# Optimization experiments

Hardware: AMD Instinct MI355X
Metric: run time of the kernel (lower is better)

The kernel has to match this reference:

```python
import jax, jax.numpy as jnp
import numpy as np
import math

B, L, D, H = 4, 1024, 1024, 16
HD = D // H

def setup_inputs() -> dict:
    rng = jax.random.key(0)
    ks = jax.random.split(rng, 11)
    def lin(k):
        # orthogonal-ish init not needed for numerics; normal scaled like torch default
        return jax.random.normal(k, (D, D), dtype=jnp.float32) * 0.02
    return {
        'key':   jax.random.normal(ks[0], (B, L, D), dtype=jnp.float32),
        'value': jax.random.normal(ks[1], (B, L, D), dtype=jnp.float32),
        'query': jax.random.normal(ks[2], (B, L, D), dtype=jnp.float32),
        'Wk': lin(ks[3]), 'bk': jnp.zeros((D,), jnp.float32),
        'Wq': lin(ks[4]), 'bq': jnp.zeros((D,), jnp.float32),
        'Wv': lin(ks[5]), 'bv': jnp.zeros((D,), jnp.float32),
        'Wp': lin(ks[6]), 'bp': jnp.zeros((D,), jnp.float32),
    }

def reference(key, value, query, Wk, bk, Wq, bq, Wv, bv, Wp, bp):
    # linear projections (torch Linear: x @ W.T + b)
    k = (key   @ Wk.T + bk).reshape(B, L, H, HD).transpose(0, 2, 1, 3)  # [B,H,L,hd]
    q = (query @ Wq.T + bq).reshape(B, L, H, HD).transpose(0, 2, 1, 3)
    v = (value @ Wv.T + bv).reshape(B, L, H, HD).transpose(0, 2, 1, 3)
    att = jnp.einsum('bhqd,bhkd->bhqk', q, k) * (1.0 / math.sqrt(HD))  # [B,H,L,L]
    causal = jnp.tril(jnp.ones((L, L), dtype=bool))
    att = jnp.where(causal[None, None], att, -jnp.inf)
    att = jax.nn.softmax(att, axis=-1)
    y = jnp.einsum('bhqk,bhkd->bhqd', att, v)  # [B,H,L,hd]
    y = y.transpose(0, 2, 1, 3).reshape(B, L, D)
    return y @ Wp.T + bp
```

## Files before the change

### kernel.cpp

```cpp
#include <hip/hip_runtime.h>

typedef unsigned short u16;
typedef __attribute__((ext_vector_type(8))) short bf16x8;
typedef __attribute__((ext_vector_type(4))) float f32x4;
typedef __attribute__((ext_vector_type(4))) unsigned short u16x4;

#define MFMA16 __builtin_amdgcn_mfma_f32_16x16x32_bf16

__device__ inline u16 f2bf(float f) {
    union { float f; unsigned u; } v; v.f = f;
    return (u16)((v.u + 0x8000u) >> 16);
}

__device__ inline void gld16(const u16* g, u16* l) {
    __builtin_amdgcn_global_load_lds(
        (const __attribute__((address_space(1))) unsigned int*)g,
        (__attribute__((address_space(3))) unsigned int*)l, 16, 0, 0);
}

struct CvtArgs { const float* src[7]; u16* dst[7]; };

__global__ __launch_bounds__(256) void cvt_kernel(CvtArgs a) {
    const int bid = blockIdx.x;
    int z, local;
    if (bid < 6144) { z = bid >> 11; local = bid & 2047; }
    else            { z = 3 + ((bid - 6144) >> 9); local = (bid - 6144) & 511; }
    const size_t i = ((size_t)local * 256 + threadIdx.x) * 8;
    const float* s = a.src[z];
    float4 v0 = *(const float4*)(s + i);
    float4 v1 = *(const float4*)(s + i + 4);
    union { u16 h[8]; bf16x8 v; } o;
    o.h[0] = f2bf(v0.x); o.h[1] = f2bf(v0.y); o.h[2] = f2bf(v0.z); o.h[3] = f2bf(v0.w);
    o.h[4] = f2bf(v1.x); o.h[5] = f2bf(v1.y); o.h[6] = f2bf(v1.z); o.h[7] = f2bf(v1.w);
    *(bf16x8*)(a.dst[z] + i) = o.v;
}

struct GemmArgs { const u16* A; const u16* W; const float* bias; void* out; int epi; };
struct Gemm3Args { GemmArgs g[3]; };

__global__ __launch_bounds__(256, 3) void gemm_qkv(Gemm3Args ga) {
    __shared__ u16 lA[128 * 64];
    __shared__ u16 lB[128 * 64];
    const GemmArgs g = ga.g[blockIdx.z];
    const int t = threadIdx.x, wave = t >> 6, lane = t & 63;
    const int quad = lane >> 4, l16 = lane & 15;
    const int bid = blockIdx.x;
    const int mtile = (bid & 7) * 4 + (bid >> 6);
    const int ntile = (bid >> 3) & 7;
    const int rowsA = mtile * 128, rowsB = ntile * 128;
    const int wm = (wave >> 1) * 64, wn = (wave & 1) * 64;
    const u16* A = g.A; const u16* W = g.W;

    f32x4 acc[4][4] = {};

    for (int kb = 0; kb < 1024; kb += 64) {
#pragma unroll
        for (int i = 0; i < 4; i++) {
            int u = (i * 4 + wave) * 64 + lane;
            int row = u >> 3, cu = (u & 7) ^ (row & 7);
            gld16(A + (size_t)(rowsA + row) * 1024 + kb + cu * 8, lA + u * 8);
        }
#pragma unroll
        for (int i = 0; i < 4; i++) {
            int u = (i * 4 + wave) * 64 + lane;
            int row = u >> 3, cu = (u & 7) ^ (row & 7);
            gld16(W + (size_t)(rowsB + row) * 1024 + kb + cu * 8, lB + u * 8);
        }
        __syncthreads();

        bf16x8 af[4][2], bfr[4][2];
#pragma unroll
        for (int mi = 0; mi < 4; mi++) {
            int row = wm + mi * 16 + l16;
#pragma unroll
            for (int kr = 0; kr < 2; kr++)
                af[mi][kr] = *(const bf16x8*)(lA + row * 64 + (((kr * 4 + quad) ^ (row & 7)) * 8));
        }
#pragma unroll
        for (int ni = 0; ni < 4; ni++) {
            int row = wn + ni * 16 + l16;
#pragma unroll
            for (int kr = 0; kr < 2; kr++)
                bfr[ni][kr] = *(const bf16x8*)(lB + row * 64 + (((kr * 4 + quad) ^ (row & 7)) * 8));
        }
#pragma unroll
        for (int mi = 0; mi < 4; mi++)
#pragma unroll
            for (int ni = 0; ni < 4; ni++) {
                acc[mi][ni] = MFMA16(af[mi][0], bfr[ni][0], acc[mi][ni], 0, 0, 0);
                acc[mi][ni] = MFMA16(af[mi][1], bfr[ni][1], acc[mi][ni], 0, 0, 0);
            }
        __syncthreads();
    }

    const int epi = g.epi;
#pragma unroll
    for (int ni = 0; ni < 4; ni++) {
        const int ncol = rowsB + wn + ni * 16 + l16;
        const float bv = g.bias[ncol];
        const int h = ncol >> 6, hd = ncol & 63;
#pragma unroll
        for (int mi = 0; mi < 4; mi++) {
            const int mrow0 = rowsA + wm + mi * 16 + quad * 4;
            const int b = mrow0 >> 10, l0 = mrow0 & 1023;
            if (epi == 0) {
#pragma unroll
                for (int r = 0; r < 4; r++)
                    ((u16*)g.out)[((size_t)(b * 16 + h) * 1024 + l0 + r) * 64 + hd] =
                        f2bf(acc[mi][ni][r] + bv);
            } else {
                u16x4 pk;
#pragma unroll
                for (int r = 0; r < 4; r++) pk[r] = f2bf(acc[mi][ni][r] + bv);
                *(u16x4*)((u16*)g.out + ((size_t)(b * 16 + h) * 64 + hd) * 1024 + l0) = pk;
            }
        }
    }
}

__global__ __launch_bounds__(256, 3) void gemm_p(const u16* __restrict__ A,
                                                 const u16* __restrict__ W,
                                                 const float* __restrict__ bias,
                                                 float* __restrict__ out)
{
    __shared__ u16 lA[128 * 64];
    __shared__ u16 lB[128 * 64];
    const int t = threadIdx.x, wave = t >> 6, lane = t & 63;
    const int quad = lane >> 4, l16 = lane & 15;
    const int bid = blockIdx.x;
    const int mtile = (bid & 7) * 4 + (bid >> 6);
    const int ntile = (bid >> 3) & 7;
    const int rowsA = mtile * 128, rowsB = ntile * 128;
    const int wm = (wave >> 1) * 64, wn = (wave & 1) * 64;

    f32x4 acc[4][4] = {};

    for (int kb = 0; kb < 1024; kb += 64) {
#pragma unroll
        for (int i = 0; i < 4; i++) {
            int u = (i * 4 + wave) * 64 + lane;
            int row = u >> 3, cu = (u & 7) ^ (row & 7);
            gld16(A + (size_t)(rowsA + row) * 1024 + kb + cu * 8, lA + u * 8);
        }
#pragma unroll
        for (int i = 0; i < 4; i++) {
            int u = (i * 4 + wave) * 64 + lane;
            int row = u >> 3, cu = (u & 7) ^ (row & 7);
            gld16(W + (size_t)(rowsB + row) * 1024 + kb + cu * 8, lB + u * 8);
        }
        __syncthreads();

        bf16x8 af[4][2], bfr[4][2];
#pragma unroll
        for (int mi = 0; mi < 4; mi++) {
            int row = wm + mi * 16 + l16;
#pragma unroll
            for (int kr = 0; kr < 2; kr++)
                af[mi][kr] = *(const bf16x8*)(lA + row * 64 + (((kr * 4 + quad) ^ (row & 7)) * 8));
        }
#pragma unroll
        for (int ni = 0; ni < 4; ni++) {
            int row = wn + ni * 16 + l16;
#pragma unroll
            for (int kr = 0; kr < 2; kr++)
                bfr[ni][kr] = *(const bf16x8*)(lB + row * 64 + (((kr * 4 + quad) ^ (row & 7)) * 8));
        }
#pragma unroll
        for (int mi = 0; mi < 4; mi++)
#pragma unroll
            for (int ni = 0; ni < 4; ni++) {
                acc[mi][ni] = MFMA16(af[mi][0], bfr[ni][0], acc[mi][ni], 0, 0, 0);
                acc[mi][ni] = MFMA16(af[mi][1], bfr[ni][1], acc[mi][ni], 0, 0, 0);
            }
        __syncthreads();
    }

#pragma unroll
    for (int ni = 0; ni < 4; ni++) {
        const int ncol = rowsB + wn + ni * 16 + l16;
        const float bv = bias[ncol];
#pragma unroll
        for (int mi = 0; mi < 4; mi++) {
            const int mrow0 = rowsA + wm + mi * 16 + quad * 4;
#pragma unroll
            for (int r = 0; r < 4; r++)
                out[(size_t)(mrow0 + r) * 1024 + ncol] = acc[mi][ni][r] + bv;
        }
    }
}

__global__ __launch_bounds__(256, 2) void attn_kernel(const u16* __restrict__ qh,
                                                      const u16* __restrict__ kh,
                                                      const u16* __restrict__ vhT,
                                                      u16* __restrict__ y)
{
    __shared__ u16 sK[2][64 * 64];
    __shared__ u16 sVT[2][64 * 64];
    __shared__ u16 sP[4 * 16 * 72];

    const int t = threadIdx.x, wave = t >> 6, lane = t & 63;
    const int quad = lane >> 4, l16 = lane & 15;
    const int bid = blockIdx.x;
    const int bh = (bid & 7) * 8 + ((bid >> 3) & 7);
    const int pr = bid >> 6;
    const int qbaseA = pr * 64 + wave * 16;
    const int qbaseB = (15 - pr) * 64 + wave * 16;
    const size_t base = (size_t)bh * 1024 * 64;
    const float e2 = 0.18033688f;

    bf16x8 aqA[2], aqB[2];
#pragma unroll
    for (int kr = 0; kr < 2; kr++) {
        aqA[kr] = *(const bf16x8*)(qh + base + (size_t)(qbaseA + l16) * 64 + kr * 32 + quad * 8);
        aqB[kr] = *(const bf16x8*)(qh + base + (size_t)(qbaseB + l16) * 64 + kr * 32 + quad * 8);
    }

    bf16x8 ones;
#pragma unroll
    for (int j = 0; j < 8; j++) ones[j] = (short)0x3F80;

    f32x4 oA[4] = {}, oB[4] = {};
    f32x4 laccA = {}, laccB = {};
    u16* pw = sP + wave * 16 * 72;

    auto STAGE = [&](int kb, int b) {
        const int krow0 = kb * 64;
#pragma unroll
        for (int i = 0; i < 2; i++) {
            int u = (i * 4 + wave) * 64 + lane;
            int row = u >> 3, cu = (u & 7) ^ (row & 7);
            gld16(kh + base + (size_t)(krow0 + row) * 64 + cu * 8, &sK[b][0] + u * 8);
        }
#pragma unroll
        for (int i = 0; i < 2; i++) {
            int u = (i * 4 + wave) * 64 + lane;
            int row = u >> 3, cu = (u & 7) ^ (row & 7);
            gld16(vhT + ((size_t)(bh * 64 + row)) * 1024 + krow0 + cu * 8, &sVT[b][0] + u * 8);
        }
    };

    STAGE(0, 0);
    __syncthreads();

    const int last = 15 - pr;
    int cur = 0;
    for (int kb = 0; kb <= last; kb++) {
        if (kb < last) STAGE(kb + 1, cur ^ 1);
        const int krow0 = kb * 64;
        const bool actA = (kb <= pr);
        const u16* sKc = sK[cur];
        const u16* sVc = sVT[cur];

        bf16x8 bk[4][2];
#pragma unroll
        for (int kc = 0; kc < 4; kc++) {
            int row = kc * 16 + l16;
#pragma unroll
            for (int kr = 0; kr < 2; kr++)
                bk[kc][kr] = *(const bf16x8*)(sKc + row * 64 + (((kr * 4 + quad) ^ (row & 7)) * 8));
        }
        f32x4 scA[4], scB[4];
        __builtin_amdgcn_s_setprio(1);
#pragma unroll
        for (int kc = 0; kc < 4; kc++) {
            f32x4 z = {};
            z = MFMA16(aqB[0], bk[kc][0], z, 0, 0, 0);
            z = MFMA16(aqB[1], bk[kc][1], z, 0, 0, 0);
            scB[kc] = z;
        }
        if (actA) {
#pragma unroll
            for (int kc = 0; kc < 4; kc++) {
                f32x4 z = {};
                z = MFMA16(aqA[0], bk[kc][0], z, 0, 0, 0);
                z = MFMA16(aqA[1], bk[kc][1], z, 0, 0, 0);
                scA[kc] = z;
            }
        }
        __builtin_amdgcn_s_setprio(0);

        bf16x8 apA0, apA1, apB0, apB1;
        if (actA) {
            const bool dmA = (krow0 + 63 > qbaseA);
#pragma unroll
            for (int kc = 0; kc < 4; kc++)
#pragma unroll
                for (int r = 0; r < 4; r++) {
                    float xv = fminf(scA[kc][r] * e2, 43.f);
                    float pv = exp2f(xv);
                    if (dmA) {
                        int kcol = krow0 + kc * 16 + l16;
                        int qrow = qbaseA + quad * 4 + r;
                        if (kcol > qrow) pv = 0.f;
                    }
                    pw[(quad * 4 + r) * 72 + kc * 16 + l16] = f2bf(pv);
                }
            apA0 = *(const bf16x8*)(pw + l16 * 72 + quad * 8);
            apA1 = *(const bf16x8*)(pw + l16 * 72 + 32 + quad * 8);
        }
        {
            const bool dmB = (krow0 + 63 > qbaseB);
#pragma unroll
            for (int kc = 0; kc < 4; kc++)
#pragma unroll
                for (int r = 0; r < 4; r++) {
                    float xv = fminf(scB[kc][r] * e2, 43.f);
                    float pv = exp2f(xv);
                    if (dmB) {
                        int kcol = krow0 + kc * 16 + l16;
                        int qrow = qbaseB + quad * 4 + r;
                        if (kcol > qrow) pv = 0.f;
                    }
                    pw[(quad * 4 + r) * 72 + kc * 16 + l16] = f2bf(pv);
                }
            apB0 = *(const bf16x8*)(pw + l16 * 72 + quad * 8);
            apB1 = *(const bf16x8*)(pw + l16 * 72 + 32 + quad * 8);
        }

        bf16x8 bv[4][2];
#pragma unroll
        for (int nt = 0; nt < 4; nt++) {
            int row = nt * 16 + l16;
#pragma unroll
            for (int kr = 0; kr < 2; kr++)
                bv[nt][kr] = *(const bf16x8*)(sVc + row * 64 + (((kr * 4 + quad) ^ (row & 7)) * 8));
        }
        __builtin_amdgcn_s_setprio(1);
#pragma unroll
        for (int nt = 0; nt < 4; nt++) {
            oB[nt] = MFMA16(apB0, bv[nt][0], oB[nt], 0, 0, 0);
            oB[nt] = MFMA16(apB1, bv[nt][1], oB[nt], 0, 0, 0);
        }
        laccB = MFMA16(apB0, ones, laccB, 0, 0, 0);
        laccB = MFMA16(apB1, ones, laccB, 0, 0, 0);
        if (actA) {
#pragma unroll
            for (int nt = 0; nt < 4; nt++) {
                oA[nt] = MFMA16(apA0, bv[nt][0], oA[nt], 0, 0, 0);
                oA[nt] = MFMA16(apA1, bv[nt][1], oA[nt], 0, 0, 0);
            }
            laccA = MFMA16(apA0, ones, laccA, 0, 0, 0);
            laccA = MFMA16(apA1, ones, laccA, 0, 0, 0);
        }
        __builtin_amdgcn_s_setprio(0);
        __syncthreads();
        cur ^= 1;
    }

    const int b = bh >> 4, h = bh & 15;
#pragma unroll
    for (int nt = 0; nt < 4; nt++)
#pragma unroll
        for (int r = 0; r < 4; r++) {
            int d = nt * 16 + l16;
            int qrA = qbaseA + quad * 4 + r;
            int qrB = qbaseB + quad * 4 + r;
            y[(size_t)(b * 1024 + qrA) * 1024 + h * 64 + d] = f2bf(oA[nt][r] / laccA[r]);
            y[(size_t)(b * 1024 + qrB) * 1024 + h * 64 + d] = f2bf(oB[nt][r] / laccB[r]);
        }
}

extern "C" void kernel_launch(void* const* d_in, const int* in_sizes, int n_in,
                              void* d_out, int out_size, void* d_ws, size_t ws_size,
                              hipStream_t stream)
{
    const float* key   = (const float*)d_in[0];
    const float* value = (const float*)d_in[1];
    const float* query = (const float*)d_in[2];
    const float* Wk = (const float*)d_in[3];
    const float* bk = (const float*)d_in[4];
    const float* Wq = (const float*)d_in[5];
    const float* bq = (const float*)d_in[6];
    const float* Wv = (const float*)d_in[7];
    const float* bv = (const float*)d_in[8];
    const float* Wp = (const float*)d_in[9];
    const float* bp = (const float*)d_in[10];

    char* ws = (char*)d_ws;
    u16* xq  = (u16*)(ws + (size_t)( 0 << 20));
    u16* xk  = (u16*)(ws + (size_t)( 8 << 20));
    u16* xv  = (u16*)(ws + (size_t)(16 << 20));
    u16* wqb = (u16*)(ws + (size_t)(24 << 20));
    u16* wkb = (u16*)(ws + (size_t)(26 << 20));
    u16* wvb = (u16*)(ws + (size_t)(28 << 20));
    u16* wpb = (u16*)(ws + (size_t)(30 << 20));
    u16* qh  = (u16*)(ws + (size_t)(32 << 20));
    u16* kh  = (u16*)(ws + (size_t)(40 << 20));
    u16* vhT = (u16*)(ws + (size_t)(48 << 20));
    u16* y   = xq;

    CvtArgs ca;
    ca.src[0] = query; ca.dst[0] = xq;
    ca.src[1] = key;   ca.dst[1] = xk;
    ca.src[2] = value; ca.dst[2] = xv;
    ca.src[3] = Wq;    ca.dst[3] = wqb;
    ca.src[4] = Wk;    ca.dst[4] = wkb;
    ca.src[5] = Wv;    ca.dst[5] = wvb;
    ca.src[6] = Wp;    ca.dst[6] = wpb;
    hipLaunchKernelGGL(cvt_kernel, dim3(8192), dim3(256), 0, stream, ca);

    Gemm3Args g3;
    g3.g[0] = GemmArgs{xq, wqb, bq, (void*)qh,  0};
    g3.g[1] = GemmArgs{xk, wkb, bk, (void*)kh,  0};
    g3.g[2] = GemmArgs{xv, wvb, bv, (void*)vhT, 2};
    hipLaunchKernelGGL(gemm_qkv, dim3(256, 1, 3), dim3(256), 0, stream, g3);

    hipLaunchKernelGGL(attn_kernel, dim3(512), dim3(256), 0, stream, qh, kh, vhT, y);

    hipLaunchKernelGGL(gemm_p, dim3(256), dim3(256), 0, stream, y, wpb, bp, (float*)d_out);
}
```

Measured before the change: 195.1 us.

## Double-buffer QKV GEMM with 256x256 tiles and interleaved prefetch

Rewrites the fused QKV projection GEMM to use 256x256 output tiles and 512 threads (8 waves, each 128x64). LDS is double-buffered so loads for the next K-slice are issued in chunks between the MFMA groups of the current slice, and s_setprio raises wave priority around the MFMA bursts. The aim is to hide global-to-LDS latency and raise operand reuse per load. The cost is 128 KB of LDS per block, which allows only one block per CU, and only 192 blocks in the grid, so some CUs may sit idle.

```diff
diff --git a/kernel.cpp b/kernel.cpp
--- a/kernel.cpp
+++ b/kernel.cpp
@@ -38,59 +38,76 @@
 struct GemmArgs { const u16* A; const u16* W; const float* bias; void* out; int epi; };
 struct Gemm3Args { GemmArgs g[3]; };
 
-__global__ __launch_bounds__(256, 3) void gemm_qkv(Gemm3Args ga) {
-    __shared__ u16 lA[128 * 64];
-    __shared__ u16 lB[128 * 64];
+__global__ __launch_bounds__(512, 2) void gemm_qkv(Gemm3Args ga) {
+    __shared__ u16 lA[2][256 * 64];
+    __shared__ u16 lB[2][256 * 64];
     const GemmArgs g = ga.g[blockIdx.z];
-    const int t = threadIdx.x, wave = t >> 6, lane = t & 63;
+    const int tid = threadIdx.x, wave = tid >> 6, lane = tid & 63;
     const int quad = lane >> 4, l16 = lane & 15;
     const int bid = blockIdx.x;
-    const int mtile = (bid & 7) * 4 + (bid >> 6);
-    const int ntile = (bid >> 3) & 7;
-    const int rowsA = mtile * 128, rowsB = ntile * 128;
-    const int wm = (wave >> 1) * 64, wn = (wave & 1) * 64;
+    const int mtile = (bid & 7) * 2 + (bid >> 5);
+    const int ntile = (bid >> 3) & 3;
+    const int rowsA = mtile * 256, rowsB = ntile * 256;
+    const int wm = (wave >> 2) * 128, wn = (wave & 3) * 64;
     const u16* A = g.A; const u16* W = g.W;
 
-    f32x4 acc[4][4] = {};
-
-    for (int kb = 0; kb < 1024; kb += 64) {
-#pragma unroll
-        for (int i = 0; i < 4; i++) {
-            int u = (i * 4 + wave) * 64 + lane;
-            int row = u >> 3, cu = (u & 7) ^ (row & 7);
-            gld16(A + (size_t)(rowsA + row) * 1024 + kb + cu * 8, lA + u * 8);
-        }
-#pragma unroll
-        for (int i = 0; i < 4; i++) {
-            int u = (i * 4 + wave) * 64 + lane;
-            int row = u >> 3, cu = (u & 7) ^ (row & 7);
-            gld16(W + (size_t)(rowsB + row) * 1024 + kb + cu * 8, lB + u * 8);
+    f32x4 acc[8][4] = {};
+
+#pragma unroll
+    for (int i = 0; i < 4; i++) {
+        int u = i * 512 + tid;
+        int row = u >> 3, cu = (u & 7) ^ (row & 7);
+        gld16(A + (size_t)(rowsA + row) * 1024 + cu * 8, &lA[0][0] + u * 8);
+        gld16(W + (size_t)(rowsB + row) * 1024 + cu * 8, &lB[0][0] + u * 8);
+    }
+    __syncthreads();
+
+    int cur = 0;
+    for (int t = 0; t < 16; t++) {
+        const int kb_next = (t + 1) * 64;
+        const bool more = (t + 1 < 16);
+        u16* nA = &lA[cur ^ 1][0]; u16* nB = &lB[cur ^ 1][0];
+        const u16* cA = &lA[cur][0]; const u16* cB = &lB[cur][0];
+
+        bf16x8 af[4][2], bfr[2][2];
+#pragma unroll
+        for (int s = 0; s < 4; s++) {
+            if (more) {
+                int u = s * 512 + tid;
+                int row = u >> 3, cu = (u & 7) ^ (row & 7);
+                gld16(A + (size_t)(rowsA + row) * 1024 + kb_next + cu * 8, nA + u * 8);
+                gld16(W + (size_t)(rowsB + row) * 1024 + kb_next + cu * 8, nB + u * 8);
+            }
+            const int miG = s >> 1, niG = s & 1;
+            if (niG == 0) {
+#pragma unroll
+                for (int mi = 0; mi < 4; mi++) {
+                    int row = wm + (miG * 4 + mi) * 16 + l16;
+#pragma unroll
+                    for (int kk = 0; kk < 2; kk++)
+                        af[mi][kk] = *(const bf16x8*)(cA + row * 64 + (((kk * 4 + quad) ^ (row & 7)) * 8));
+                }
+            }
+#pragma unroll
+            for (int ni = 0; ni < 2; ni++) {
+                int row = wn + (niG * 2 + ni) * 16 + l16;
+#pragma unroll
+                for (int kk = 0; kk < 2; kk++)
+                    bfr[ni][kk] = *(const bf16x8*)(cB + row * 64 + (((kk * 4 + quad) ^ (row & 7)) * 8));
+            }
+            __builtin_amdgcn_s_setprio(1);
+#pragma unroll
+            for (int mi = 0; mi < 4; mi++)
+#pragma unroll
+                for (int ni = 0; ni < 2; ni++) {
+                    f32x4& a = acc[miG * 4 + mi][niG * 2 + ni];
+                    a = MFMA16(af[mi][0], bfr[ni][0], a, 0, 0, 0);
+                    a = MFMA16(af[mi][1], bfr[ni][1], a, 0, 0, 0);
+                }
+            __builtin_amdgcn_s_setprio(0);
         }
         __syncthreads();
-
-        bf16x8 af[4][2], bfr[4][2];
-#pragma unroll
-        for (int mi = 0; mi < 4; mi++) {
-            int row = wm + mi * 16 + l16;
-#pragma unroll
-            for (int kr = 0; kr < 2; kr++)
-                af[mi][kr] = *(const bf16x8*)(lA + row * 64 + (((kr * 4 + quad) ^ (row & 7)) * 8));
-        }
-#pragma unroll
-        for (int ni = 0; ni < 4; ni++) {
-            int row = wn + ni * 16 + l16;
-#pragma unroll
-            for (int kr = 0; kr < 2; kr++)
-                bfr[ni][kr] = *(const bf16x8*)(lB + row * 64 + (((kr * 4 + quad) ^ (row & 7)) * 8));
-        }
-#pragma unroll
-        for (int mi = 0; mi < 4; mi++)
-#pragma unroll
-            for (int ni = 0; ni < 4; ni++) {
-                acc[mi][ni] = MFMA16(af[mi][0], bfr[ni][0], acc[mi][ni], 0, 0, 0);
-                acc[mi][ni] = MFMA16(af[mi][1], bfr[ni][1], acc[mi][ni], 0, 0, 0);
-            }
-        __syncthreads();
+        cur ^= 1;
     }
 
     const int epi = g.epi;
@@ -100,7 +117,7 @@
         const float bv = g.bias[ncol];
         const int h = ncol >> 6, hd = ncol & 63;
 #pragma unroll
-        for (int mi = 0; mi < 4; mi++) {
+        for (int mi = 0; mi < 8; mi++) {
             const int mrow0 = rowsA + wm + mi * 16 + quad * 4;
             const int b = mrow0 >> 10, l0 = mrow0 & 1023;
             if (epi == 0) {
@@ -403,7 +420,7 @@
     g3.g[0] = GemmArgs{xq, wqb, bq, (void*)qh,  0};
     g3.g[1] = GemmArgs{xk, wkb, bk, (void*)kh,  0};
     g3.g[2] = GemmArgs{xv, wvb, bv, (void*)vhT, 2};
-    hipLaunchKernelGGL(gemm_qkv, dim3(256, 1, 3), dim3(256), 0, stream, g3);
+    hipLaunchKernelGGL(gemm_qkv, dim3(64, 1, 3), dim3(512), 0, stream, g3);
 
     hipLaunchKernelGGL(attn_kernel, dim3(512), dim3(256), 0, stream, qh, kh, vhT, y);
 
```

Result: slower. 211.4 us (+8.3%).

## Double-buffer LDS in projection GEMMs with interleaved async loads and MFMA

Applied to the files above, without the earlier changes.

Both the QKV and output projection GEMMs now keep two LDS buffers and prefetch the next K-tile with global_load_lds while computing on the current one. The loads are split into quarter chunks placed between sub-tile MFMA groups, using explicit vmcnt waits, raw barriers and sched fences in place of full __syncthreads. MFMA sections are also raised in priority with setprio. The aim is to hide global-memory latency behind compute. In exchange LDS use doubles and occupancy falls from 3 to 2 blocks per CU, and the hand-placed wait counts must exactly match the outstanding loads.

```diff
diff --git a/kernel.cpp b/kernel.cpp
--- a/kernel.cpp
+++ b/kernel.cpp
@@ -6,6 +6,9 @@
 typedef __attribute__((ext_vector_type(4))) unsigned short u16x4;
 
 #define MFMA16 __builtin_amdgcn_mfma_f32_16x16x32_bf16
+#define VMCNT(n) asm volatile("s_waitcnt vmcnt(" #n ")" ::: "memory")
+#define SFENCE() __builtin_amdgcn_sched_barrier(0)
+#define RBAR() __builtin_amdgcn_s_barrier()
 
 __device__ inline u16 f2bf(float f) {
     union { float f; unsigned u; } v; v.f = f;
@@ -38,9 +41,9 @@
 struct GemmArgs { const u16* A; const u16* W; const float* bias; void* out; int epi; };
 struct Gemm3Args { GemmArgs g[3]; };
 
-__global__ __launch_bounds__(256, 3) void gemm_qkv(Gemm3Args ga) {
-    __shared__ u16 lA[128 * 64];
-    __shared__ u16 lB[128 * 64];
+__global__ __launch_bounds__(256, 2) void gemm_qkv(Gemm3Args ga) {
+    __shared__ u16 lA[2][128 * 64];
+    __shared__ u16 lB[2][128 * 64];
     const GemmArgs g = ga.g[blockIdx.z];
     const int t = threadIdx.x, wave = t >> 6, lane = t & 63;
     const int quad = lane >> 4, l16 = lane & 15;
@@ -52,45 +55,78 @@
     const u16* A = g.A; const u16* W = g.W;
 
     f32x4 acc[4][4] = {};
-
-    for (int kb = 0; kb < 1024; kb += 64) {
-#pragma unroll
-        for (int i = 0; i < 4; i++) {
+    bf16x8 af[2][2], bfr[2][2];
+
+    auto ISSUE = [&](const u16* src, int rows0, int kb, int q, u16* dst) {
+#pragma unroll
+        for (int j = 0; j < 2; j++) {
+            int i = q + j * 2;
             int u = (i * 4 + wave) * 64 + lane;
             int row = u >> 3, cu = (u & 7) ^ (row & 7);
-            gld16(A + (size_t)(rowsA + row) * 1024 + kb + cu * 8, lA + u * 8);
-        }
-#pragma unroll
-        for (int i = 0; i < 4; i++) {
-            int u = (i * 4 + wave) * 64 + lane;
-            int row = u >> 3, cu = (u & 7) ^ (row & 7);
-            gld16(W + (size_t)(rowsB + row) * 1024 + kb + cu * 8, lB + u * 8);
-        }
-        __syncthreads();
-
-        bf16x8 af[4][2], bfr[4][2];
-#pragma unroll
-        for (int mi = 0; mi < 4; mi++) {
-            int row = wm + mi * 16 + l16;
-#pragma unroll
-            for (int kr = 0; kr < 2; kr++)
-                af[mi][kr] = *(const bf16x8*)(lA + row * 64 + (((kr * 4 + quad) ^ (row & 7)) * 8));
-        }
-#pragma unroll
-        for (int ni = 0; ni < 4; ni++) {
-            int row = wn + ni * 16 + l16;
-#pragma unroll
-            for (int kr = 0; kr < 2; kr++)
-                bfr[ni][kr] = *(const bf16x8*)(lB + row * 64 + (((kr * 4 + quad) ^ (row & 7)) * 8));
-        }
-#pragma unroll
-        for (int mi = 0; mi < 4; mi++)
-#pragma unroll
-            for (int ni = 0; ni < 4; ni++) {
-                acc[mi][ni] = MFMA16(af[mi][0], bfr[ni][0], acc[mi][ni], 0, 0, 0);
-                acc[mi][ni] = MFMA16(af[mi][1], bfr[ni][1], acc[mi][ni], 0, 0, 0);
+            gld16(src + (size_t)(rows0 + row) * 1024 + kb + cu * 8, dst + u * 8);
+        }
+    };
+    auto RD_A = [&](const u16* cbuf, int miG) {
+#pragma unroll
+        for (int mi = 0; mi < 2; mi++) {
+            int row = wm + miG * 32 + mi * 16 + l16;
+#pragma unroll
+            for (int kk = 0; kk < 2; kk++)
+                af[mi][kk] = *(const bf16x8*)(cbuf + row * 64 + (((kk * 4 + quad) ^ (row & 7)) * 8));
+        }
+    };
+    auto RD_B = [&](const u16* cbuf, int niG) {
+#pragma unroll
+        for (int ni = 0; ni < 2; ni++) {
+            int row = wn + niG * 32 + ni * 16 + l16;
+#pragma unroll
+            for (int kk = 0; kk < 2; kk++)
+                bfr[ni][kk] = *(const bf16x8*)(cbuf + row * 64 + (((kk * 4 + quad) ^ (row & 7)) * 8));
+        }
+    };
+    auto MM = [&](int miG, int niG) {
+        __builtin_amdgcn_s_setprio(1);
+#pragma unroll
+        for (int mi = 0; mi < 2; mi++)
+#pragma unroll
+            for (int ni = 0; ni < 2; ni++) {
+                f32x4& a = acc[miG * 2 + mi][niG * 2 + ni];
+                a = MFMA16(af[mi][0], bfr[ni][0], a, 0, 0, 0);
+                a = MFMA16(af[mi][1], bfr[ni][1], a, 0, 0, 0);
             }
-        __syncthreads();
+        __builtin_amdgcn_s_setprio(0);
+    };
+
+    ISSUE(A, rowsA, 0, 0, lA[0]); ISSUE(W, rowsB, 0, 0, lB[0]);
+    ISSUE(A, rowsA, 0, 1, lA[0]); ISSUE(W, rowsB, 0, 1, lB[0]);
+    VMCNT(4); RBAR(); SFENCE();
+
+    int c = 0;
+    for (int tt = 0; tt < 15; tt++) {
+        const int kbn = (tt + 1) * 64;
+        const u16* cA = lA[c]; const u16* cB = lB[c];
+        u16* nA = lA[c ^ 1]; u16* nB = lB[c ^ 1];
+        ISSUE(A, rowsA, kbn, 0, nA);
+        RD_A(cA, 0); RD_B(cB, 0); MM(0, 0);
+        VMCNT(4); RBAR(); SFENCE();
+        ISSUE(W, rowsB, kbn, 0, nB);
+        RD_A(cA, 1); MM(1, 0);
+        VMCNT(4); RBAR(); SFENCE();
+        ISSUE(A, rowsA, kbn, 1, nA);
+        RD_B(cB, 1); MM(1, 1);
+        ISSUE(W, rowsB, kbn, 1, nB);
+        RD_A(cA, 0); MM(0, 1);
+        VMCNT(4); RBAR(); SFENCE();
+        c ^= 1;
+    }
+    {
+        const u16* cA = lA[c]; const u16* cB = lB[c];
+        RD_A(cA, 0); RD_B(cB, 0); MM(0, 0);
+        VMCNT(2); RBAR(); SFENCE();
+        RD_A(cA, 1); MM(1, 0);
+        VMCNT(0); RBAR(); SFENCE();
+        RD_B(cB, 1); MM(1, 1);
+        RD_A(cA, 0); MM(0, 1);
     }
 
     const int epi = g.epi;
@@ -118,13 +154,13 @@
     }
 }
 
-__global__ __launch_bounds__(256, 3) void gemm_p(const u16* __restrict__ A,
+__global__ __launch_bounds__(256, 2) void gemm_p(const u16* __restrict__ A,
                                                  const u16* __restrict__ W,
                                                  const float* __restrict__ bias,
                                                  float* __restrict__ out)
 {
-    __shared__ u16 lA[128 * 64];
-    __shared__ u16 lB[128 * 64];
+    __shared__ u16 lA[2][128 * 64];
+    __shared__ u16 lB[2][128 * 64];
     const int t = threadIdx.x, wave = t >> 6, lane = t & 63;
     const int quad = lane >> 4, l16 = lane & 15;
     const int bid = blockIdx.x;
@@ -134,45 +170,78 @@
     const int wm = (wave >> 1) * 64, wn = (wave & 1) * 64;
 
     f32x4 acc[4][4] = {};
-
-    for (int kb = 0; kb < 1024; kb += 64) {
-#pragma unroll
-        for (int i = 0; i < 4; i++) {
+    bf16x8 af[2][2], bfr[2][2];
+
+    auto ISSUE = [&](const u16* src, int rows0, int kb, int q, u16* dst) {
+#pragma unroll
+        for (int j = 0; j < 2; j++) {
+            int i = q + j * 2;
             int u = (i * 4 + wave) * 64 + lane;
             int row = u >> 3, cu = (u & 7) ^ (row & 7);
-            gld16(A + (size_t)(rowsA + row) * 1024 + kb + cu * 8, lA + u * 8);
-        }
-#pragma unroll
-        for (int i = 0; i < 4; i++) {
-            int u = (i * 4 + wave) * 64 + lane;
-            int row = u >> 3, cu = (u & 7) ^ (row & 7);
-            gld16(W + (size_t)(rowsB + row) * 1024 + kb + cu * 8, lB + u * 8);
-        }
-        __syncthreads();
-
-        bf16x8 af[4][2], bfr[4][2];
-#pragma unroll
-        for (int mi = 0; mi < 4; mi++) {
-            int row = wm + mi * 16 + l16;
-#pragma unroll
-            for (int kr = 0; kr < 2; kr++)
-                af[mi][kr] = *(const bf16x8*)(lA + row * 64 + (((kr * 4 + quad) ^ (row & 7)) * 8));
-        }
-#pragma unroll
-        for (int ni = 0; ni < 4; ni++) {
-            int row = wn + ni * 16 + l16;
-#pragma unroll
-            for (int kr = 0; kr < 2; kr++)
-                bfr[ni][kr] = *(const bf16x8*)(lB + row * 64 + (((kr * 4 + quad) ^ (row & 7)) * 8));
-        }
-#pragma unroll
-        for (int mi = 0; mi < 4; mi++)
-#pragma unroll
-            for (int ni = 0; ni < 4; ni++) {
-                acc[mi][ni] = MFMA16(af[mi][0], bfr[ni][0], acc[mi][ni], 0, 0, 0);
-                acc[mi][ni] = MFMA16(af[mi][1], bfr[ni][1], acc[mi][ni], 0, 0, 0);
+            gld16(src + (size_t)(rows0 + row) * 1024 + kb + cu * 8, dst + u * 8);
+        }
+    };
+    auto RD_A = [&](const u16* cbuf, int miG) {
+#pragma unroll
+        for (int mi = 0; mi < 2; mi++) {
+            int row = wm + miG * 32 + mi * 16 + l16;
+#pragma unroll
+            for (int kk = 0; kk < 2; kk++)
+                af[mi][kk] = *(const bf16x8*)(cbuf + row * 64 + (((kk * 4 + quad) ^ (row & 7)) * 8));
+        }
+    };
+    auto RD_B = [&](const u16* cbuf, int niG) {
+#pragma unroll
+        for (int ni = 0; ni < 2; ni++) {
+            int row = wn + niG * 32 + ni * 16 + l16;
+#pragma unroll
+            for (int kk = 0; kk < 2; kk++)
+                bfr[ni][kk] = *(const bf16x8*)(cbuf + row * 64 + (((kk * 4 + quad) ^ (row & 7)) * 8));
+        }
+    };
+    auto MM = [&](int miG, int niG) {
+        __builtin_amdgcn_s_setprio(1);
+#pragma unroll
+        for (int mi = 0; mi < 2; mi++)
+#pragma unroll
+            for (int ni = 0; ni < 2; ni++) {
+                f32x4& a = acc[miG * 2 + mi][niG * 2 + ni];
+                a = MFMA16(af[mi][0], bfr[ni][0], a, 0, 0, 0);
+                a = MFMA16(af[mi][1], bfr[ni][1], a, 0, 0, 0);
             }
-        __syncthreads();
+        __builtin_amdgcn_s_setprio(0);
+    };
+
+    ISSUE(A, rowsA, 0, 0, lA[0]); ISSUE(W, rowsB, 0, 0, lB[0]);
+    ISSUE(A, rowsA, 0, 1, lA[0]); ISSUE(W, rowsB, 0, 1, lB[0]);
+    VMCNT(4); RBAR(); SFENCE();
+
+    int c = 0;
+    for (int tt = 0; tt < 15; tt++) {
+        const int kbn = (tt + 1) * 64;
+        const u16* cA = lA[c]; const u16* cB = lB[c];
+        u16* nA = lA[c ^ 1]; u16* nB = lB[c ^ 1];
+        ISSUE(A, rowsA, kbn, 0, nA);
+        RD_A(cA, 0); RD_B(cB, 0); MM(0, 0);
+        VMCNT(4); RBAR(); SFENCE();
+        ISSUE(W, rowsB, kbn, 0, nB);
+        RD_A(cA, 1); MM(1, 0);
+        VMCNT(4); RBAR(); SFENCE();
+        ISSUE(A, rowsA, kbn, 1, nA);
+        RD_B(cB, 1); MM(1, 1);
+        ISSUE(W, rowsB, kbn, 1, nB);
+        RD_A(cA, 0); MM(0, 1);
+        VMCNT(4); RBAR(); SFENCE();
+        c ^= 1;
+    }
+    {
+        const u16* cA = lA[c]; const u16* cB = lB[c];
+        RD_A(cA, 0); RD_B(cB, 0); MM(0, 0);
+        VMCNT(2); RBAR(); SFENCE();
+        RD_A(cA, 1); MM(1, 0);
+        VMCNT(0); RBAR(); SFENCE();
+        RD_B(cB, 1); MM(1, 1);
+        RD_A(cA, 0); MM(0, 1);
     }
 
 #pragma unroll
```

Result: slower. 217.6 us (+11.5%).
